# Kernel optimization log

Hardware: AMD Instinct MI355X
Metric: run time of the kernel (lower is better)

Reference implementation:

```python
import jax, jax.numpy as jnp
import numpy as np

N_HEAD = 16
D_MODEL = 1024
D_HEAD = D_MODEL // N_HEAD
B, T = 2, 2048


def setup_inputs() -> dict:
    key = jax.random.key(0)
    k1, k2, k3 = jax.random.split(key, 3)
    x = jax.random.normal(k1, (B, T, D_MODEL), dtype=jnp.float32)
    w_attn = jax.random.normal(k2, (3 * D_MODEL, D_MODEL), dtype=jnp.float32) * (D_MODEL ** -0.5)
    w_proj = jax.random.normal(k3, (D_MODEL, D_MODEL), dtype=jnp.float32) * (D_MODEL ** -0.5)
    return {"x": x, "w_attn": w_attn, "w_proj": w_proj}


def _rms_norm(x):
    eps = jnp.asarray(jnp.finfo(x.dtype).eps, x.dtype)
    var = jnp.mean(jnp.square(x), axis=-1, keepdims=True)
    return x * jax.lax.rsqrt(var + eps)


def _rotate_half(x):
    x1, x2 = jnp.split(x, 2, axis=-1)
    return jnp.concatenate((-x2, x1), axis=-1)


def reference(x, w_attn, w_proj):
    Bx, Tx, C = x.shape
    qkv = jnp.einsum('btc,fc->btf', x, w_attn)  # [B,T,3C]
    q, k, v = jnp.split(qkv, 3, axis=-1)
    # [B, H, T, Dh]
    q = q.reshape(Bx, Tx, N_HEAD, D_HEAD).transpose(0, 2, 1, 3)
    k = k.reshape(Bx, Tx, N_HEAD, D_HEAD).transpose(0, 2, 1, 3)
    v = v.reshape(Bx, Tx, N_HEAD, D_HEAD).transpose(0, 2, 1, 3)
    # QK RMSNorm (no learned weight)
    q = _rms_norm(q)
    k = _rms_norm(k)
    # Rotary embedding over full d_head: freqs tiled twice
    inv_freq = 1.0 / (10000.0 ** (jnp.arange(0, D_HEAD, 2, dtype=jnp.float32) / D_HEAD))
    t = jnp.arange(Tx, dtype=jnp.float32)
    freqs = jnp.einsum('i,j->ij', t, inv_freq)  # [T, Dh/2]
    emb = jnp.concatenate((freqs, freqs), axis=-1)  # [T, Dh]
    cos = jnp.cos(emb)[None, None, :, :]
    sin = jnp.sin(emb)[None, None, :, :]
    q = q * cos + _rotate_half(q) * sin
    k = k * cos + _rotate_half(k) * sin
    # Causal SDPA
    scale = D_HEAD ** -0.5
    scores = jnp.einsum('bhqd,bhkd->bhqk', q, k) * scale
    causal = jnp.tril(jnp.ones((Tx, Tx), dtype=bool))
    scores = jnp.where(causal[None, None], scores, jnp.asarray(-jnp.inf, scores.dtype))
    attn = jax.nn.softmax(scores, axis=-1)
    y = jnp.einsum('bhqk,bhkd->bhqd', attn, v)
    y = y.transpose(0, 2, 1, 3).reshape(Bx, Tx, C)
    return jnp.einsum('btc,oc->bto', y, w_proj)
```

## Files before the change

### kernel.cpp

```cpp
#include <hip/hip_runtime.h>
#include <cstdint>
#include <cstddef>


typedef short bf16x8 __attribute__((ext_vector_type(8)));
typedef float floatx4 __attribute__((ext_vector_type(4)));
typedef unsigned short ushortx8 __attribute__((ext_vector_type(8)));
typedef unsigned short ushortx4 __attribute__((ext_vector_type(4)));
typedef unsigned int uintx2 __attribute__((ext_vector_type(2)));

#define DEVI __device__ __forceinline__

DEVI float bf2f(unsigned short u) {
    unsigned int x = ((unsigned int)u) << 16;
    return __builtin_bit_cast(float, x);
}
DEVI unsigned short f2bf(float f) {
    unsigned int u = __builtin_bit_cast(unsigned int, f);
    u += 0x7fffu + ((u >> 16) & 1u);
    return (unsigned short)(u >> 16);
}
DEVI unsigned int pkbf2(float a, float b) {
    unsigned int ua = __builtin_bit_cast(unsigned int, a) + 0x8000u;
    unsigned int ub = __builtin_bit_cast(unsigned int, b) + 0x8000u;
    return __builtin_amdgcn_perm(ub, ua, 0x07060302);
}

DEVI void glds16(const unsigned short* g, unsigned short* l) {
    __builtin_amdgcn_global_load_lds(
        (const __attribute__((address_space(1))) unsigned int*)g,
        (__attribute__((address_space(3))) unsigned int*)l, 16, 0, 0);
}

DEVI void cast8(unsigned short* dst, const float* src) {
    floatx4 a = *(const floatx4*)src;
    floatx4 b = *(const floatx4*)(src + 4);
    ushortx8 o;
    o[0] = f2bf(a[0]); o[1] = f2bf(a[1]); o[2] = f2bf(a[2]); o[3] = f2bf(a[3]);
    o[4] = f2bf(b[0]); o[5] = f2bf(b[1]); o[6] = f2bf(b[2]); o[7] = f2bf(b[3]);
    *(ushortx8*)dst = o;
}

__global__ __launch_bounds__(256)
void cast_inputs(const float* __restrict__ x, const float* __restrict__ wa,
                 const float* __restrict__ wp,
                 unsigned short* __restrict__ xb, unsigned short* __restrict__ wab,
                 unsigned short* __restrict__ wpb)
{
    size_t g = (size_t)blockIdx.x * 256 + threadIdx.x;
    size_t stride = (size_t)gridDim.x * 256;
    for (size_t i = g; i < (4194304 / 8); i += stride) cast8(xb  + i * 8, x  + i * 8);
    for (size_t i = g; i < (3145728 / 8); i += stride) cast8(wab + i * 8, wa + i * 8);
    for (size_t i = g; i < (1048576 / 8); i += stride) cast8(wpb + i * 8, wp + i * 8);
}

__global__ __launch_bounds__(512, 2)
void gemm_qkv_8ph(const unsigned short* __restrict__ A,
                  const unsigned short* __restrict__ B,
                  unsigned short* __restrict__ Cqk,
                  unsigned short* __restrict__ Vt)
{
    __shared__ __align__(16) unsigned short lds[2][2][256 * 64];

    const int tid  = threadIdx.x;
    const int lane = tid & 63;
    const int w    = tid >> 6;
    const int wm   = w >> 2;
    const int wn   = w & 3;
    const int quad = lane >> 4;
    const int lm   = lane & 15;

    const int lin = blockIdx.y * 12 + blockIdx.x;
    const int s   = (lin & 7) * 24 + (lin >> 3);
    const int m0  = (s / 12) * 256;
    const int n0  = (s % 12) * 256;

    const int srow = tid >> 3;
    const int scol = ((tid & 7) * 8) ^ (((tid >> 5) & 1) << 4);
    const int ldst = w * 512;

#define STG_A(u, WBi, kq) glds16(&A[(size_t)(m0 + (u) * 64 + srow) * 1024 + (kq) + scol], \
                                 &lds[WBi][0][(u) * 4096 + ldst])
#define STG_B(u, WBi, kq) glds16(&B[(size_t)(n0 + (u) * 64 + srow) * 1024 + (kq) + scol], \
                                 &lds[WBi][1][(u) * 4096 + ldst])
#define RD_A(RBi, rrow, off) (*(const bf16x8*)&lds[RBi][0][(((rrow) * 64 + (off))) ^ ((((rrow) >> 2) & 1) << 4)])
#define RD_B(RBi, rrow, off) (*(const bf16x8*)&lds[RBi][1][(((rrow) * 64 + (off))) ^ ((((rrow) >> 2) & 1) << 4)])

    floatx4 acc[8][4] = {};
    bf16x8 afr[4][2];
    bf16x8 bfr[4][2];

#define MQ(MB, JB)                                                              \
  do {                                                                          \
    _Pragma("unroll")                                                           \
    for (int kk = 0; kk < 2; ++kk)                                              \
      _Pragma("unroll")                                                         \
      for (int mi = 0; mi < 4; ++mi)                                            \
        _Pragma("unroll")                                                       \
        for (int j2 = 0; j2 < 2; ++j2)                                          \
          acc[(MB) + mi][(JB) + j2] = __builtin_amdgcn_mfma_f32_16x16x32_bf16(  \
              afr[mi][kk], bfr[(JB) + j2][kk], acc[(MB) + mi][(JB) + j2], 0, 0, 0); \
  } while (0)

#define TILE(RBi, WBi, KT, LASTF)                                               \
  do {                                                                          \
    const int kn = ((KT) + 1) * 64;                                             \
               \
    _Pragma("unroll")                                                           \
    for (int kk = 0; kk < 2; ++kk) {                                            \
      _Pragma("unroll")                                                         \
      for (int mi = 0; mi < 4; ++mi)                                            \
        afr[mi][kk] = RD_A(RBi, wm * 128 + mi * 16 + lm, kk * 32 + quad * 8);   \
      _Pragma("unroll")                                                         \
      for (int j2 = 0; j2 < 2; ++j2)                                            \
        bfr[j2][kk] = RD_B(RBi, wn * 64 + j2 * 16 + lm, kk * 32 + quad * 8);    \
    }                                                                           \
    if (!(LASTF)) { STG_B(0, WBi, kn); STG_B(1, WBi, kn); }                     \
    __builtin_amdgcn_s_barrier();                                               \
    asm volatile("s_waitcnt lgkmcnt(0)" ::: "memory");                          \
    __builtin_amdgcn_s_setprio(1); MQ(0, 0); __builtin_amdgcn_s_setprio(0);     \
    __builtin_amdgcn_s_barrier();                                               \
              \
    _Pragma("unroll")                                                           \
    for (int kk = 0; kk < 2; ++kk)                                              \
      _Pragma("unroll")                                                         \
      for (int j2 = 0; j2 < 2; ++j2)                                            \
        bfr[2 + j2][kk] = RD_B(RBi, wn * 64 + (2 + j2) * 16 + lm, kk * 32 + quad * 8); \
    if (!(LASTF)) { STG_B(2, WBi, kn); STG_B(3, WBi, kn);                       \
                    asm volatile("s_waitcnt vmcnt(4)" ::: "memory"); }          \
    else          { asm volatile("s_waitcnt vmcnt(0)" ::: "memory"); }          \
    __builtin_amdgcn_s_barrier();                                               \
    asm volatile("s_waitcnt lgkmcnt(0)" ::: "memory");                          \
    __builtin_amdgcn_s_setprio(1); MQ(0, 2); __builtin_amdgcn_s_setprio(0);     \
    __builtin_amdgcn_s_barrier();                                               \
                          \
    _Pragma("unroll")                                                           \
    for (int kk = 0; kk < 2; ++kk)                                              \
      _Pragma("unroll")                                                         \
      for (int mi = 0; mi < 4; ++mi)                                            \
        afr[mi][kk] = RD_A(RBi, wm * 128 + 64 + mi * 16 + lm, kk * 32 + quad * 8); \
    if (!(LASTF)) { STG_A(0, WBi, kn); STG_A(2, WBi, kn); }                     \
    __builtin_amdgcn_s_barrier();                                               \
    asm volatile("s_waitcnt lgkmcnt(0)" ::: "memory");                          \
    __builtin_amdgcn_s_setprio(1); MQ(4, 2); __builtin_amdgcn_s_setprio(0);     \
    __builtin_amdgcn_s_barrier();                                               \
      \
    if (!(LASTF)) { STG_A(1, WBi, kn); STG_A(3, WBi, kn);                       \
                    asm volatile("s_waitcnt vmcnt(2)" ::: "memory"); }          \
    __builtin_amdgcn_s_barrier();                                               \
    __builtin_amdgcn_s_setprio(1); MQ(4, 0); __builtin_amdgcn_s_setprio(0);     \
    __builtin_amdgcn_s_barrier();                                               \
  } while (0)

    STG_B(0, 0, 0); STG_B(1, 0, 0); STG_B(2, 0, 0); STG_B(3, 0, 0);
    STG_A(0, 0, 0); STG_A(2, 0, 0); STG_A(1, 0, 0); STG_A(3, 0, 0);
    asm volatile("s_waitcnt vmcnt(2)" ::: "memory");
    __builtin_amdgcn_s_barrier();

    for (int kt = 0; kt < 14; kt += 2) {
        TILE(0, 1, kt, false);
        TILE(1, 0, kt + 1, false);
    }
    TILE(0, 1, 14, false);
    TILE(1, 0, 15, true);

    const bool is_v = (n0 + wn * 64) >= 2048;
    if (!is_v) {
        float invf[4];
        #pragma unroll
        for (int j = 0; j < 4; ++j) {
            int d = j * 16 + lm;
            invf[j] = __expf(-(float)(d & 31) * 0.28782313662425572f);
        }
        #pragma unroll
        for (int mi = 0; mi < 8; ++mi) {
            float rn[4];
            #pragma unroll
            for (int r = 0; r < 4; ++r) {
                float ss = 0.0f;
                #pragma unroll
                for (int j = 0; j < 4; ++j) ss += acc[mi][j][r] * acc[mi][j][r];
                ss += __shfl_xor(ss, 1, 64);
                ss += __shfl_xor(ss, 2, 64);
                ss += __shfl_xor(ss, 4, 64);
                ss += __shfl_xor(ss, 8, 64);
                rn[r] = rsqrtf(ss * (1.0f / 64.0f) + 1.1920929e-07f);
            }
            #pragma unroll
            for (int r = 0; r < 4; ++r) {
                int row = m0 + wm * 128 + mi * 16 + quad * 4 + r;
                float t = (float)(row & 2047);
                float g = rn[r];
                #pragma unroll
                for (int j = 0; j < 4; ++j) {
                    int d = j * 16 + lm;
                    float sn, cs;
                    __sincosf(t * invf[j], &sn, &cs);
                    float v  = acc[mi][j][r] * g;
                    float vp = acc[mi][j ^ 2][r] * g;
                    float sgn = (d < 32) ? -1.0f : 1.0f;
                    Cqk[(size_t)row * 2048 + (n0 + wn * 64 + d)] =
                        f2bf(v * cs + sgn * vp * sn);
                }
            }
        }
    } else {
        #pragma unroll
        for (int mi = 0; mi < 8; ++mi)
            #pragma unroll
            for (int j = 0; j < 4; ++j) {
                int col  = n0 + wn * 64 + j * 16 + lm;
                int row0 = m0 + wm * 128 + mi * 16 + quad * 4;
                int bq = row0 >> 11, t0 = row0 & 2047;
                ushortx4 pk;
                #pragma unroll
                for (int r = 0; r < 4; ++r) pk[r] = f2bf(acc[mi][j][r]);
                *(ushortx4*)&Vt[((size_t)(bq * 1024 + (col - 2048))) * 2048 + t0] = pk;
            }
    }
#undef TILE
#undef MQ
#undef RD_A
#undef RD_B
#undef STG_A
#undef STG_B
}

template <bool QKV_SPLIT, int BN, int BK>
__global__ __launch_bounds__(256)
void gemm_bt(const unsigned short* __restrict__ A, const unsigned short* __restrict__ B,
             unsigned short* __restrict__ Cqk, float* __restrict__ Cf,
             unsigned short* __restrict__ Vt, int M, int N, int K)
{
    constexpr int WCOLS = (BN == 128) ? 2 : 1;
    constexpr int WROWS = 4 / WCOLS;
    constexpr int MI    = 128 / (16 * WROWS);
    constexpr int LPR   = BK / 8;
    constexpr int RPI   = 64 / LPR;

    __shared__ __align__(16) unsigned short As[128 * BK];
    __shared__ __align__(16) unsigned short Bs[BN * BK];

    const int tid  = threadIdx.x;
    const int lane = tid & 63;
    const int w    = tid >> 6;
    const int wm   = w / WCOLS, wn = w % WCOLS;
    const int quad = lane >> 4;
    const int lm   = lane & 15;
    const int m0 = blockIdx.y * 128;
    const int n0 = blockIdx.x * BN;
    const int sr = lane / LPR;
    const int sc = (lane % LPR) * 8;

    floatx4 acc[MI][4] = {};

    for (int k0 = 0; k0 < K; k0 += BK) {
        __syncthreads();
        #pragma unroll
        for (int i = 0; i < 32 / RPI; ++i) {
            int r = w * 32 + i * RPI;
            glds16(&A[(size_t)(m0 + r + sr) * K + k0 + sc], &As[r * BK]);
        }
        #pragma unroll
        for (int i = 0; i < (BN / 4) / RPI; ++i) {
            int r = w * (BN / 4) + i * RPI;
            glds16(&B[(size_t)(n0 + r + sr) * K + k0 + sc], &Bs[r * BK]);
        }
        __syncthreads();

        #pragma unroll
        for (int kk = 0; kk < BK / 32; ++kk) {
            bf16x8 a[MI];
            #pragma unroll
            for (int i = 0; i < MI; ++i)
                a[i] = *(const bf16x8*)&As[(wm * (16 * MI) + i * 16 + lm) * BK + kk * 32 + quad * 8];
            #pragma unroll
            for (int j = 0; j < 4; ++j) {
                bf16x8 b = *(const bf16x8*)&Bs[(wn * 64 + j * 16 + lm) * BK + kk * 32 + quad * 8];
                #pragma unroll
                for (int i = 0; i < MI; ++i)
                    acc[i][j] = __builtin_amdgcn_mfma_f32_16x16x32_bf16(a[i], b, acc[i][j], 0, 0, 0);
            }
        }
    }

    if constexpr (QKV_SPLIT) {
        const bool is_v = (n0 + wn * 64) >= 2048;
        if (!is_v) {
            float rn[MI][4];
            #pragma unroll
            for (int i = 0; i < MI; ++i)
                #pragma unroll
                for (int r = 0; r < 4; ++r) {
                    float s = 0.0f;
                    #pragma unroll
                    for (int j = 0; j < 4; ++j) s += acc[i][j][r] * acc[i][j][r];
                    s += __shfl_xor(s, 1, 64);
                    s += __shfl_xor(s, 2, 64);
                    s += __shfl_xor(s, 4, 64);
                    s += __shfl_xor(s, 8, 64);
                    rn[i][r] = rsqrtf(s * (1.0f / 64.0f) + 1.1920929e-07f);
                }
            float invf[4];
            #pragma unroll
            for (int j = 0; j < 4; ++j) {
                int d = j * 16 + lm;
                invf[j] = __expf(-(float)(d & 31) * 0.28782313662425572f);
            }
            #pragma unroll
            for (int i = 0; i < MI; ++i)
                #pragma unroll
                for (int r = 0; r < 4; ++r) {
                    int row = m0 + wm * (16 * MI) + i * 16 + quad * 4 + r;
                    float t = (float)(row & 2047);
                    float g = rn[i][r];
                    #pragma unroll
                    for (int j = 0; j < 4; ++j) {
                        int d = j * 16 + lm;
                        float sn, cs;
                        __sincosf(t * invf[j], &sn, &cs);
                        float v  = acc[i][j][r] * g;
                        float vp = acc[i][j ^ 2][r] * g;
                        float sgn = (d < 32) ? -1.0f : 1.0f;
                        Cqk[(size_t)row * 2048 + (n0 + wn * 64 + d)] =
                            f2bf(v * cs + sgn * vp * sn);
                    }
                }
        } else {
            #pragma unroll
            for (int i = 0; i < MI; ++i)
                #pragma unroll
                for (int j = 0; j < 4; ++j) {
                    int col  = n0 + wn * 64 + j * 16 + lm;
                    int row0 = m0 + wm * (16 * MI) + i * 16 + quad * 4;
                    int bq = row0 >> 11, t0 = row0 & 2047;
                    ushortx4 pk;
                    #pragma unroll
                    for (int r = 0; r < 4; ++r) pk[r] = f2bf(acc[i][j][r]);
                    *(ushortx4*)&Vt[((size_t)(bq * 1024 + (col - 2048))) * 2048 + t0] = pk;
                }
        }
    } else {
        #pragma unroll
        for (int i = 0; i < MI; ++i)
            #pragma unroll
            for (int j = 0; j < 4; ++j) {
                int col  = n0 + wn * 64 + j * 16 + lm;
                int row0 = m0 + wm * (16 * MI) + i * 16 + quad * 4;
                #pragma unroll
                for (int r = 0; r < 4; ++r)
                    Cf[(size_t)(row0 + r) * N + col] = acc[i][j][r];
            }
    }
}

#define ATTN_STEP(KSc, VSc, KSn, VSn, KT, DG, LAST)                            \
  do {                                                                         \
    if (!(LAST)) {                                                             \
      *(ushortx8*)&(KSn)[r0 * LD + pc] = kreg0;                                \
      *(ushortx8*)&(KSn)[r1 * LD + pc] = kreg1;                                \
      *(ushortx8*)&(VSn)[r0 * LD + pc] = vreg0;                                \
      *(ushortx8*)&(VSn)[r1 * LD + pc] = vreg1;                                \
      if ((KT) + 2 <= qt) {                                                    \
        kreg0 = *(const ushortx8*)kp0; kreg1 = *(const ushortx8*)kp1;          \
        vreg0 = *(const ushortx8*)vp0; vreg1 = *(const ushortx8*)vp1;          \
        kp0 += (size_t)64 * 2048; kp1 += (size_t)64 * 2048;                    \
        vp0 += 64; vp1 += 64;                                                  \
      }                                                                        \
    }                                                                          \
    floatx4 sa[4] = {};                                                        \
    _Pragma("unroll")                                                          \
    for (int kk = 0; kk < 2; ++kk)                                             \
      _Pragma("unroll")                                                        \
      for (int j = 0; j < 4; ++j) {                                            \
        bf16x8 kf = *(const bf16x8*)&(KSc)[(j * 16 + lm) * LD + kk * 32 + quad * 8]; \
        sa[j] = __builtin_amdgcn_mfma_f32_16x16x32_bf16(kf, qf[kk], sa[j], 0, 0, 0); \
      }                                                                        \
    _Pragma("unroll")                                                          \
    for (int j = 0; j < 4; ++j) {                                              \
      float p0 = exp2f(sa[j][0] * c1 - c2);                                    \
      float p1 = exp2f(sa[j][1] * c1 - c2);                                    \
      float p2 = exp2f(sa[j][2] * c1 - c2);                                    \
      float p3 = exp2f(sa[j][3] * c1 - c2);                                    \
      if (DG) {                                                                \
        int kb = (KT) * 64 + j * 16 + quad * 4;                                \
        if (kb + 0 > qrow) p0 = 0.0f;                                          \
        if (kb + 1 > qrow) p1 = 0.0f;                                          \
        if (kb + 2 > qrow) p2 = 0.0f;                                          \
        if (kb + 3 > qrow) p3 = 0.0f;                                          \
      }                                                                        \
      uintx2 pk;                                                               \
      pk[0] = pkbf2(p0, p1);                                                   \
      pk[1] = pkbf2(p2, p3);                                                   \
      *(uintx2*)&QPs[(w * 16 + lm) * LD + j * 16 + quad * 4] = pk;             \
    }                                                                          \
    _Pragma("unroll")                                                          \
    for (int kk = 0; kk < 2; ++kk) {                                           \
      bf16x8 pf = *(const bf16x8*)&QPs[(w * 16 + lm) * LD + kk * 32 + quad * 8]; \
      _Pragma("unroll")                                                        \
      for (int j = 0; j < 4; ++j) {                                            \
        bf16x8 vf = *(const bf16x8*)&(VSc)[(j * 16 + lm) * LD + kk * 32 + quad * 8]; \
        o[j] = __builtin_amdgcn_mfma_f32_16x16x32_bf16(pf, vf, o[j], 0, 0, 0); \
      }                                                                        \
      l_acc = __builtin_amdgcn_mfma_f32_16x16x32_bf16(pf, ones, l_acc, 0, 0, 0); \
    }                                                                          \
    if (!(LAST)) __syncthreads();                                              \
  } while (0)

__global__ __launch_bounds__(256)
void attention(const unsigned short* __restrict__ qk,
               const unsigned short* __restrict__ Vt,
               unsigned short* __restrict__ Y)
{
    constexpr int LD = 72;
    __shared__ __align__(16) unsigned short QPs[64 * LD];
    __shared__ __align__(16) unsigned short Ks0[64 * LD];
    __shared__ __align__(16) unsigned short Ks1[64 * LD];
    __shared__ __align__(16) unsigned short Vs0[64 * LD];
    __shared__ __align__(16) unsigned short Vs1[64 * LD];

    const int tid  = threadIdx.x;
    const int lane = tid & 63;
    const int w    = tid >> 6;
    const int quad = lane >> 4;
    const int lm   = lane & 15;

    const int bh = blockIdx.x;
    const int qt = 31 - blockIdx.y;
    const int b  = bh >> 4, h = bh & 15;
    const int q0 = qt * 64;
    const int qrow = q0 + w * 16 + lm;

    const int r0 = tid >> 3, r1 = r0 + 32, pc = (tid & 7) * 8;
    const unsigned short* kp0 = qk + (size_t)b * 2048 * 2048 + 1024 + h * 64
                              + (size_t)r0 * 2048 + pc;
    const unsigned short* kp1 = kp0 + (size_t)32 * 2048;
    const unsigned short* vp0 = Vt + (size_t)bh * 64 * 2048 + (size_t)r0 * 2048 + pc;
    const unsigned short* vp1 = vp0 + (size_t)32 * 2048;

    #pragma unroll
    for (int i = 0; i < 2; ++i) {
        int c = i * 256 + tid, row = c >> 3, col = (c & 7) * 8;
        *(ushortx8*)&QPs[row * LD + col] =
            *(const ushortx8*)&qk[((size_t)(b * 2048 + q0 + row)) * 2048 + h * 64 + col];
    }

    ushortx8 kreg0 = *(const ushortx8*)kp0, kreg1 = *(const ushortx8*)kp1;
    ushortx8 vreg0 = *(const ushortx8*)vp0, vreg1 = *(const ushortx8*)vp1;
    kp0 += (size_t)64 * 2048; kp1 += (size_t)64 * 2048;
    vp0 += 64; vp1 += 64;
    *(ushortx8*)&Ks0[r0 * LD + pc] = kreg0;
    *(ushortx8*)&Ks0[r1 * LD + pc] = kreg1;
    *(ushortx8*)&Vs0[r0 * LD + pc] = vreg0;
    *(ushortx8*)&Vs0[r1 * LD + pc] = vreg1;
    if (qt >= 1) {
        kreg0 = *(const ushortx8*)kp0; kreg1 = *(const ushortx8*)kp1;
        vreg0 = *(const ushortx8*)vp0; vreg1 = *(const ushortx8*)vp1;
        kp0 += (size_t)64 * 2048; kp1 += (size_t)64 * 2048;
        vp0 += 64; vp1 += 64;
    }
    __syncthreads();

    bf16x8 qf[2];
    #pragma unroll
    for (int kk = 0; kk < 2; ++kk)
        qf[kk] = *(const bf16x8*)&QPs[(w * 16 + lm) * LD + kk * 32 + quad * 8];

    bf16x8 ones;
    #pragma unroll
    for (int i = 0; i < 8; ++i) ones[i] = (short)0x3F80;

    floatx4 o[4] = {};
    floatx4 l_acc = {};
    const float c1 = 0.125f * 1.44269504f;
    const float c2 = 8.0f   * 1.44269504f;

    int kt = 0;
    for (; kt + 1 < qt; kt += 2) {
        ATTN_STEP(Ks0, Vs0, Ks1, Vs1, kt,     false, false);
        ATTN_STEP(Ks1, Vs1, Ks0, Vs0, kt + 1, false, false);
    }
    if (kt < qt) {
        ATTN_STEP(Ks0, Vs0, Ks1, Vs1, kt, false, false);
        ATTN_STEP(Ks1, Vs1, Ks0, Vs0, qt, true, true);
    } else {
        ATTN_STEP(Ks0, Vs0, Ks1, Vs1, qt, true, true);
    }

    float rinv[4];
    #pragma unroll
    for (int r = 0; r < 4; ++r) rinv[r] = 1.0f / l_acc[r];

    #pragma unroll
    for (int j = 0; j < 4; ++j) {
        int colg = h * 64 + j * 16 + lm;
        #pragma unroll
        for (int r = 0; r < 4; ++r) {
            int rowg = q0 + w * 16 + quad * 4 + r;
            Y[((size_t)(b * 2048 + rowg)) * 1024 + colg] = f2bf(o[j][r] * rinv[r]);
        }
    }
}

extern "C" void kernel_launch(void* const* d_in, const int* in_sizes, int n_in,
                              void* d_out, int out_size, void* d_ws, size_t ws_size,
                              hipStream_t stream)
{
    const float* x      = (const float*)d_in[0];
    const float* w_attn = (const float*)d_in[1];
    const float* w_proj = (const float*)d_in[2];
    float* out = (float*)d_out;

    unsigned short* qkbuf = (unsigned short*)d_ws;
    unsigned short* Vtb   = qkbuf + (size_t)4096 * 2048;
    unsigned short* y     = Vtb   + (size_t)32 * 64 * 2048;
    unsigned short* wpb   = y     + (size_t)4096 * 1024;
    unsigned short* xb  = (unsigned short*)d_out;
    unsigned short* wab = xb + (size_t)4096 * 1024;

    dim3 blk(256);
    cast_inputs<<<dim3(1024), blk, 0, stream>>>(x, w_attn, w_proj, xb, wab, wpb);
    gemm_qkv_8ph<<<dim3(12, 16), dim3(512), 0, stream>>>(xb, wab, qkbuf, Vtb);
    attention<<<dim3(32, 32), blk, 0, stream>>>(qkbuf, Vtb, y);
    gemm_bt<false, 64, 64>
        <<<dim3(16, 32), blk, 0, stream>>>(y, wpb, nullptr, out, nullptr, 4096, 1024, 1024);
}
```

Before: 185.5 us.

## Precompute rotary table, use full XOR LDS swizzle, reorder QKV GEMM stages

The cast kernel now also fills a cos/sin rotary table, and the QKV GEMM epilogue reads it instead of computing sincos per element. The GEMM's LDS layout switches from a 2-way XOR swizzle to an 8-way XOR swizzle on 16-byte chunks, aimed at fewer bank conflicts on fragment reads. Global-to-LDS stage issues move ahead of the LDS reads, with a partial lgkmcnt wait, for more load/compute overlap. The unused QKV_SPLIT epilogue in the generic GEMM template is removed. This adds a small table build and extra global reads in the epilogue, and the table sits in scratch space inside the output buffer.

```diff
diff --git a/kernel.cpp b/kernel.cpp
--- a/kernel.cpp
+++ b/kernel.cpp
@@ -5,6 +5,7 @@
 
 typedef short bf16x8 __attribute__((ext_vector_type(8)));
 typedef float floatx4 __attribute__((ext_vector_type(4)));
+typedef float floatx2 __attribute__((ext_vector_type(2)));
 typedef unsigned short ushortx8 __attribute__((ext_vector_type(8)));
 typedef unsigned short ushortx4 __attribute__((ext_vector_type(4)));
 typedef unsigned int uintx2 __attribute__((ext_vector_type(2)));
@@ -45,18 +46,27 @@
 void cast_inputs(const float* __restrict__ x, const float* __restrict__ wa,
                  const float* __restrict__ wp,
                  unsigned short* __restrict__ xb, unsigned short* __restrict__ wab,
-                 unsigned short* __restrict__ wpb)
+                 unsigned short* __restrict__ wpb, float* __restrict__ ropetab)
 {
     size_t g = (size_t)blockIdx.x * 256 + threadIdx.x;
     size_t stride = (size_t)gridDim.x * 256;
     for (size_t i = g; i < (4194304 / 8); i += stride) cast8(xb  + i * 8, x  + i * 8);
     for (size_t i = g; i < (3145728 / 8); i += stride) cast8(wab + i * 8, wa + i * 8);
     for (size_t i = g; i < (1048576 / 8); i += stride) cast8(wpb + i * 8, wp + i * 8);
+    for (size_t i = g; i < 65536; i += stride) {
+        int t = (int)(i >> 5), f = (int)(i & 31);
+        float ang = (float)t * __expf(-(float)f * 0.28782313662425572f);
+        float sn, cs;
+        __sincosf(ang, &sn, &cs);
+        ropetab[2 * i]     = cs;
+        ropetab[2 * i + 1] = sn;
+    }
 }
 
 __global__ __launch_bounds__(512, 2)
 void gemm_qkv_8ph(const unsigned short* __restrict__ A,
                   const unsigned short* __restrict__ B,
+                  const float* __restrict__ ropetab,
                   unsigned short* __restrict__ Cqk,
                   unsigned short* __restrict__ Vt)
 {
@@ -76,15 +86,15 @@
     const int n0  = (s % 12) * 256;
 
     const int srow = tid >> 3;
-    const int scol = ((tid & 7) * 8) ^ (((tid >> 5) & 1) << 4);
+    const int scol = (((tid & 7) ^ ((tid >> 3) & 7)) * 8);
     const int ldst = w * 512;
 
 #define STG_A(u, WBi, kq) glds16(&A[(size_t)(m0 + (u) * 64 + srow) * 1024 + (kq) + scol], \
                                  &lds[WBi][0][(u) * 4096 + ldst])
 #define STG_B(u, WBi, kq) glds16(&B[(size_t)(n0 + (u) * 64 + srow) * 1024 + (kq) + scol], \
                                  &lds[WBi][1][(u) * 4096 + ldst])
-#define RD_A(RBi, rrow, off) (*(const bf16x8*)&lds[RBi][0][(((rrow) * 64 + (off))) ^ ((((rrow) >> 2) & 1) << 4)])
-#define RD_B(RBi, rrow, off) (*(const bf16x8*)&lds[RBi][1][(((rrow) * 64 + (off))) ^ ((((rrow) >> 2) & 1) << 4)])
+#define RD_A(RBi, rrow, kk) (*(const bf16x8*)&lds[RBi][0][(rrow) * 64 + ((((kk) * 4 + quad) ^ ((rrow) & 7)) * 8)])
+#define RD_B(RBi, rrow, kk) (*(const bf16x8*)&lds[RBi][1][(rrow) * 64 + ((((kk) * 4 + quad) ^ ((rrow) & 7)) * 8)])
 
     floatx4 acc[8][4] = {};
     bf16x8 afr[4][2];
@@ -105,41 +115,42 @@
 #define TILE(RBi, WBi, KT, LASTF)                                               \
   do {                                                                          \
     const int kn = ((KT) + 1) * 64;                                             \
-               \
+                \
+    if (!(LASTF)) { STG_B(0, WBi, kn); STG_B(1, WBi, kn); }                     \
     _Pragma("unroll")                                                           \
     for (int kk = 0; kk < 2; ++kk) {                                            \
       _Pragma("unroll")                                                         \
       for (int mi = 0; mi < 4; ++mi)                                            \
-        afr[mi][kk] = RD_A(RBi, wm * 128 + mi * 16 + lm, kk * 32 + quad * 8);   \
+        afr[mi][kk] = RD_A(RBi, wm * 128 + mi * 16 + lm, kk);                   \
       _Pragma("unroll")                                                         \
       for (int j2 = 0; j2 < 2; ++j2)                                            \
-        bfr[j2][kk] = RD_B(RBi, wn * 64 + j2 * 16 + lm, kk * 32 + quad * 8);    \
+        bfr[j2][kk] = RD_B(RBi, wn * 64 + j2 * 16 + lm, kk);                    \
     }                                                                           \
-    if (!(LASTF)) { STG_B(0, WBi, kn); STG_B(1, WBi, kn); }                     \
+    asm volatile("s_waitcnt lgkmcnt(8)" ::: "memory");                          \
     __builtin_amdgcn_s_barrier();                                               \
     asm volatile("s_waitcnt lgkmcnt(0)" ::: "memory");                          \
     __builtin_amdgcn_s_setprio(1); MQ(0, 0); __builtin_amdgcn_s_setprio(0);     \
     __builtin_amdgcn_s_barrier();                                               \
-              \
+               \
+    if (!(LASTF)) { STG_B(2, WBi, kn); STG_B(3, WBi, kn); }                     \
     _Pragma("unroll")                                                           \
     for (int kk = 0; kk < 2; ++kk)                                              \
       _Pragma("unroll")                                                         \
       for (int j2 = 0; j2 < 2; ++j2)                                            \
-        bfr[2 + j2][kk] = RD_B(RBi, wn * 64 + (2 + j2) * 16 + lm, kk * 32 + quad * 8); \
-    if (!(LASTF)) { STG_B(2, WBi, kn); STG_B(3, WBi, kn);                       \
-                    asm volatile("s_waitcnt vmcnt(4)" ::: "memory"); }          \
+        bfr[2 + j2][kk] = RD_B(RBi, wn * 64 + (2 + j2) * 16 + lm, kk);          \
+    if (!(LASTF)) { asm volatile("s_waitcnt vmcnt(4)" ::: "memory"); }          \
     else          { asm volatile("s_waitcnt vmcnt(0)" ::: "memory"); }          \
     __builtin_amdgcn_s_barrier();                                               \
     asm volatile("s_waitcnt lgkmcnt(0)" ::: "memory");                          \
     __builtin_amdgcn_s_setprio(1); MQ(0, 2); __builtin_amdgcn_s_setprio(0);     \
     __builtin_amdgcn_s_barrier();                                               \
-                          \
+                           \
+    if (!(LASTF)) { STG_A(0, WBi, kn); STG_A(2, WBi, kn); }                     \
     _Pragma("unroll")                                                           \
     for (int kk = 0; kk < 2; ++kk)                                              \
       _Pragma("unroll")                                                         \
       for (int mi = 0; mi < 4; ++mi)                                            \
-        afr[mi][kk] = RD_A(RBi, wm * 128 + 64 + mi * 16 + lm, kk * 32 + quad * 8); \
-    if (!(LASTF)) { STG_A(0, WBi, kn); STG_A(2, WBi, kn); }                     \
+        afr[mi][kk] = RD_A(RBi, wm * 128 + 64 + mi * 16 + lm, kk);              \
     __builtin_amdgcn_s_barrier();                                               \
     asm volatile("s_waitcnt lgkmcnt(0)" ::: "memory");                          \
     __builtin_amdgcn_s_setprio(1); MQ(4, 2); __builtin_amdgcn_s_setprio(0);     \
@@ -166,12 +177,7 @@
 
     const bool is_v = (n0 + wn * 64) >= 2048;
     if (!is_v) {
-        float invf[4];
-        #pragma unroll
-        for (int j = 0; j < 4; ++j) {
-            int d = j * 16 + lm;
-            invf[j] = __expf(-(float)(d & 31) * 0.28782313662425572f);
-        }
+        const floatx2* rtab = (const floatx2*)ropetab;
         #pragma unroll
         for (int mi = 0; mi < 8; ++mi) {
             float rn[4];
@@ -189,13 +195,15 @@
             #pragma unroll
             for (int r = 0; r < 4; ++r) {
                 int row = m0 + wm * 128 + mi * 16 + quad * 4 + r;
-                float t = (float)(row & 2047);
+                int t = row & 2047;
+                floatx2 cs0 = rtab[t * 32 + lm];
+                floatx2 cs1 = rtab[t * 32 + 16 + lm];
                 float g = rn[r];
                 #pragma unroll
                 for (int j = 0; j < 4; ++j) {
                     int d = j * 16 + lm;
-                    float sn, cs;
-                    __sincosf(t * invf[j], &sn, &cs);
+                    float cs = (j & 1) ? cs1[0] : cs0[0];
+                    float sn = (j & 1) ? cs1[1] : cs0[1];
                     float v  = acc[mi][j][r] * g;
                     float vp = acc[mi][j ^ 2][r] * g;
                     float sgn = (d < 32) ? -1.0f : 1.0f;
@@ -285,61 +293,6 @@
     }
 
     if constexpr (QKV_SPLIT) {
-        const bool is_v = (n0 + wn * 64) >= 2048;
-        if (!is_v) {
-            float rn[MI][4];
-            #pragma unroll
-            for (int i = 0; i < MI; ++i)
-                #pragma unroll
-                for (int r = 0; r < 4; ++r) {
-                    float s = 0.0f;
-                    #pragma unroll
-                    for (int j = 0; j < 4; ++j) s += acc[i][j][r] * acc[i][j][r];
-                    s += __shfl_xor(s, 1, 64);
-                    s += __shfl_xor(s, 2, 64);
-                    s += __shfl_xor(s, 4, 64);
-                    s += __shfl_xor(s, 8, 64);
-                    rn[i][r] = rsqrtf(s * (1.0f / 64.0f) + 1.1920929e-07f);
-                }
-            float invf[4];
-            #pragma unroll
-            for (int j = 0; j < 4; ++j) {
-                int d = j * 16 + lm;
-                invf[j] = __expf(-(float)(d & 31) * 0.28782313662425572f);
-            }
-            #pragma unroll
-            for (int i = 0; i < MI; ++i)
-                #pragma unroll
-                for (int r = 0; r < 4; ++r) {
-                    int row = m0 + wm * (16 * MI) + i * 16 + quad * 4 + r;
-                    float t = (float)(row & 2047);
-                    float g = rn[i][r];
-                    #pragma unroll
-                    for (int j = 0; j < 4; ++j) {
-                        int d = j * 16 + lm;
-                        float sn, cs;
-                        __sincosf(t * invf[j], &sn, &cs);
-                        float v  = acc[i][j][r] * g;
-                        float vp = acc[i][j ^ 2][r] * g;
-                        float sgn = (d < 32) ? -1.0f : 1.0f;
-                        Cqk[(size_t)row * 2048 + (n0 + wn * 64 + d)] =
-                            f2bf(v * cs + sgn * vp * sn);
-                    }
-                }
-        } else {
-            #pragma unroll
-            for (int i = 0; i < MI; ++i)
-                #pragma unroll
-                for (int j = 0; j < 4; ++j) {
-                    int col  = n0 + wn * 64 + j * 16 + lm;
-                    int row0 = m0 + wm * (16 * MI) + i * 16 + quad * 4;
-                    int bq = row0 >> 11, t0 = row0 & 2047;
-                    ushortx4 pk;
-                    #pragma unroll
-                    for (int r = 0; r < 4; ++r) pk[r] = f2bf(acc[i][j][r]);
-                    *(ushortx4*)&Vt[((size_t)(bq * 1024 + (col - 2048))) * 2048 + t0] = pk;
-                }
-        }
     } else {
         #pragma unroll
         for (int i = 0; i < MI; ++i)
@@ -517,10 +470,11 @@
     unsigned short* wpb   = y     + (size_t)4096 * 1024;
     unsigned short* xb  = (unsigned short*)d_out;
     unsigned short* wab = xb + (size_t)4096 * 1024;
+    float* ropetab = (float*)(wab + (size_t)3072 * 1024);
 
     dim3 blk(256);
-    cast_inputs<<<dim3(1024), blk, 0, stream>>>(x, w_attn, w_proj, xb, wab, wpb);
-    gemm_qkv_8ph<<<dim3(12, 16), dim3(512), 0, stream>>>(xb, wab, qkbuf, Vtb);
+    cast_inputs<<<dim3(1024), blk, 0, stream>>>(x, w_attn, w_proj, xb, wab, wpb, ropetab);
+    gemm_qkv_8ph<<<dim3(12, 16), dim3(512), 0, stream>>>(xb, wab, ropetab, qkbuf, Vtb);
     attention<<<dim3(32, 32), blk, 0, stream>>>(qkbuf, Vtb, y);
     gemm_bt<false, 64, 64>
         <<<dim3(16, 32), blk, 0, stream>>>(y, wpb, nullptr, out, nullptr, 4096, 1024, 1024);
```

Measured after the change: 176.2 us. 5.0% less time.
